# Kernel optimization log

Hardware: AMD Instinct MI355X
Metric: run time of the kernel (lower is better)

The kernel has to match this reference:

```python
import jax, jax.numpy as jnp
import numpy as np

EMBED_DIM = 1024
NUM_HEADS = 16
HEAD_DIM = EMBED_DIM // NUM_HEADS
EPS = 1e-6
B, T = 4, 8192


def setup_inputs() -> dict:
    key = jax.random.key(0)
    ks = jax.random.split(key, 11)
    s = 1.0 / np.sqrt(EMBED_DIM)
    inp = {
        'query': jax.random.normal(ks[0], (B, T, EMBED_DIM), jnp.float32),
        'key': jax.random.normal(ks[1], (B, T, EMBED_DIM), jnp.float32),
        'value': jax.random.normal(ks[2], (B, T, EMBED_DIM), jnp.float32),
        'Wq': jax.random.normal(ks[3], (EMBED_DIM, EMBED_DIM), jnp.float32) * s,
        'bq': jnp.zeros((EMBED_DIM,), jnp.float32),
        'Wk': jax.random.normal(ks[4], (EMBED_DIM, EMBED_DIM), jnp.float32) * s,
        'bk': jnp.zeros((EMBED_DIM,), jnp.float32),
        'Wv': jax.random.normal(ks[5], (EMBED_DIM, EMBED_DIM), jnp.float32) * s,
        'bv': jnp.zeros((EMBED_DIM,), jnp.float32),
        'Wo': jax.random.normal(ks[6], (EMBED_DIM, EMBED_DIM), jnp.float32) * s,
        'bo': jnp.zeros((EMBED_DIM,), jnp.float32),
    }
    return inp


def _feature_map(x):
    return jax.nn.elu(x) + 1.0


def reference(query, key, value, Wq, bq, Wk, bk, Wv, bv, Wo, bo):
    b, t, _ = query.shape
    # projections (torch Linear: x @ W.T + b)
    q = query @ Wq.T + bq
    k = key @ Wk.T + bk
    v = value @ Wv.T + bv
    # split heads -> (b, h, t, d)
    def split(x):
        return x.reshape(b, t, NUM_HEADS, HEAD_DIM).transpose(0, 2, 1, 3)
    q = _feature_map(split(q))
    k = _feature_map(split(k))
    v = split(v)
    k_sum = k.sum(axis=2)                                   # (b,h,d)
    denom = jnp.einsum('bhtd,bhd->bht', q, k_sum) + EPS     # (b,h,t)
    kv = jnp.einsum('bhtd,bhtv->bhdv', k, v)                # (b,h,d,d)
    out = jnp.einsum('bhtd,bhde->bhte', q, kv) / denom[..., None]
    out = out.transpose(0, 2, 1, 3).reshape(b, t, EMBED_DIM)
    return out @ Wo.T + bo
```

## Files before the change

### kernel.cpp

```cpp
#include <hip/hip_runtime.h>
#include <hip/hip_bf16.h>

typedef long long TLONG;
typedef float  f32x4_t  __attribute__((ext_vector_type(4)));
typedef short  s16x8_t  __attribute__((ext_vector_type(8)));
typedef short  s16x4_t  __attribute__((ext_vector_type(4)));
typedef __bf16 bf16x8_t __attribute__((ext_vector_type(8)));

#define MDIM 32768
#define NDIM 1024
#define KDIM 1024
#define EPSV 1e-6f

__device__ __forceinline__ unsigned short f2bf_bits(float f) {
  __hip_bfloat16 h = __float2bfloat16(f);
  return __builtin_bit_cast(unsigned short, h);
}
__device__ __forceinline__ float bf2f(unsigned short u) {
  unsigned int x = ((unsigned int)u) << 16;
  return __builtin_bit_cast(float, x);
}
__device__ __forceinline__ void load_lds16(const void* g, void* l) {
  __builtin_amdgcn_global_load_lds((const __attribute__((address_space(1))) void*)g,
                                   (__attribute__((address_space(3))) void*)l, 16, 0, 0);
}

__global__ __launch_bounds__(256) void convert_f32_bf16(
    const float* __restrict__ in, unsigned short* __restrict__ out, TLONG n) {
  TLONG i = ((TLONG)blockIdx.x * blockDim.x + threadIdx.x) * 8;
  const TLONG stride = (TLONG)gridDim.x * blockDim.x * 8;
  for (; i < n; i += stride) {
    f32x4_t a = *reinterpret_cast<const f32x4_t*>(in + i);
    f32x4_t b = *reinterpret_cast<const f32x4_t*>(in + i + 4);
    s16x8_t o;
    o[0] = (short)f2bf_bits(a[0]); o[1] = (short)f2bf_bits(a[1]);
    o[2] = (short)f2bf_bits(a[2]); o[3] = (short)f2bf_bits(a[3]);
    o[4] = (short)f2bf_bits(b[0]); o[5] = (short)f2bf_bits(b[1]);
    o[6] = (short)f2bf_bits(b[2]); o[7] = (short)f2bf_bits(b[3]);
    *reinterpret_cast<s16x8_t*>(out + i) = o;
  }
}

template <int FMAP, int OUT>
__global__ __launch_bounds__(256) void gemm_bt(
    const unsigned short* __restrict__ A, const unsigned short* __restrict__ W,
    const float* __restrict__ bias, void* __restrict__ Cout) {
  const int bid = blockIdx.x;
  const int swz = (bid & 7) * 256 + (bid >> 3);
  const int mt = swz >> 3;
  const int nt = swz & 7;

  const int tid = threadIdx.x;
  const int lane = tid & 63;
  const int w = tid >> 6;
  const int wr = w >> 1, wc = w & 1;
  const int l15 = lane & 15, lh = lane >> 4;

  __shared__ short sA[128 * 32];
  __shared__ short sB[128 * 32];

  f32x4_t acc[4][4];
#pragma unroll
  for (int m = 0; m < 4; ++m)
#pragma unroll
    for (int n = 0; n < 4; ++n) acc[m][n] = (f32x4_t)0.0f;

  const int arow0 = mt * 128;
  const int brow0 = nt * 128;

  for (int kt = 0; kt < KDIM / 32; ++kt) {
    const int k0 = kt * 32;
#pragma unroll
    for (int i = 0; i < 2; ++i) {
      const int c = i * 256 + tid;
      const int r = c >> 2, s = c & 3;
      const int sg = s ^ ((r >> 1) & 3);
      load_lds16(A + ((arow0 + r) * KDIM + k0 + sg * 8), &sA[c * 8]);
    }
#pragma unroll
    for (int i = 0; i < 2; ++i) {
      const int c = i * 256 + tid;
      const int r = c >> 2, s = c & 3;
      const int sg = s ^ ((r >> 1) & 3);
      load_lds16(W + ((brow0 + r) * KDIM + k0 + sg * 8), &sB[c * 8]);
    }
    __syncthreads();
    bf16x8_t a[4], b[4];
#pragma unroll
    for (int m = 0; m < 4; ++m) {
      const int rA = wr * 64 + m * 16 + l15;
      const int sl = lh ^ ((rA >> 1) & 3);
      a[m] = __builtin_bit_cast(bf16x8_t,
          *reinterpret_cast<const s16x8_t*>(&sA[rA * 32 + sl * 8]));
    }
#pragma unroll
    for (int n = 0; n < 4; ++n) {
      const int rB = wc * 64 + n * 16 + l15;
      const int sl = lh ^ ((rB >> 1) & 3);
      b[n] = __builtin_bit_cast(bf16x8_t,
          *reinterpret_cast<const s16x8_t*>(&sB[rB * 32 + sl * 8]));
    }
#pragma unroll
    for (int m = 0; m < 4; ++m)
#pragma unroll
      for (int n = 0; n < 4; ++n)
        acc[m][n] = __builtin_amdgcn_mfma_f32_16x16x32_bf16(a[m], b[n], acc[m][n], 0, 0, 0);
    __syncthreads();
  }

#pragma unroll
  for (int n = 0; n < 4; ++n) {
    const int col = nt * 128 + wc * 64 + n * 16 + l15;
    const float bv = bias[col];
#pragma unroll
    for (int m = 0; m < 4; ++m) {
      const int row0 = mt * 128 + wr * 64 + m * 16 + lh * 4;
      if (OUT == 2) {
        const int b = row0 >> 13, tl = row0 & 8191;
        const int h = col >> 6, d = col & 63;
        s16x4_t o;
#pragma unroll
        for (int j = 0; j < 4; ++j) {
          float v = acc[m][n][j] + bv;
          if (FMAP) v = (v > 0.0f) ? (v + 1.0f) : __expf(v);
          o[j] = (short)f2bf_bits(v);
        }
        *reinterpret_cast<s16x4_t*>(
            reinterpret_cast<unsigned short*>(Cout) +
            (((b * 16 + h) * 64 + d) * 8192 + tl)) = o;
      } else {
#pragma unroll
        for (int j = 0; j < 4; ++j) {
          float v = acc[m][n][j] + bv;
          if (FMAP) v = (v > 0.0f) ? (v + 1.0f) : __expf(v);
          if (OUT == 1)
            reinterpret_cast<float*>(Cout)[(row0 + j) * NDIM + col] = v;
          else
            reinterpret_cast<unsigned short*>(Cout)[(row0 + j) * NDIM + col] = f2bf_bits(v);
        }
      }
    }
  }
}

__global__ __launch_bounds__(256) void kv_ksum_mfma(
    const unsigned short* __restrict__ kT, const unsigned short* __restrict__ vT,
    float* __restrict__ kvT, float* __restrict__ ksum) {
  const int bid = blockIdx.x;
  const int bh = bid >> 4, ch = bid & 15;
  const int tid = threadIdx.x;
  const int lane = tid & 63, w = tid >> 6;
  const int l15 = lane & 15, lh = lane >> 4;
  const int dblk = (w >> 1) * 32, eblk = (w & 1) * 32;

  f32x4_t acc[2][2];
#pragma unroll
  for (int m = 0; m < 2; ++m)
#pragma unroll
    for (int n = 0; n < 2; ++n) acc[m][n] = (f32x4_t)0.0f;
  float ks0 = 0.f, ks1 = 0.f;

  const int tbase = ch * 512 + lh * 8;
  const unsigned short* ka = kT + (bh * 64 + dblk + l15) * 8192 + tbase;
  const unsigned short* va = vT + (bh * 64 + eblk + l15) * 8192 + tbase;

  for (int t0 = 0; t0 < 512; t0 += 32) {
    s16x8_t ar[2], br[2];
#pragma unroll
    for (int m = 0; m < 2; ++m)
      ar[m] = *reinterpret_cast<const s16x8_t*>(ka + m * 16 * 8192 + t0);
#pragma unroll
    for (int n = 0; n < 2; ++n)
      br[n] = *reinterpret_cast<const s16x8_t*>(va + n * 16 * 8192 + t0);
#pragma unroll
    for (int m = 0; m < 2; ++m)
#pragma unroll
      for (int n = 0; n < 2; ++n)
        acc[m][n] = __builtin_amdgcn_mfma_f32_16x16x32_bf16(
            __builtin_bit_cast(bf16x8_t, ar[m]),
            __builtin_bit_cast(bf16x8_t, br[n]), acc[m][n], 0, 0, 0);
    if (eblk == 0) {
#pragma unroll
      for (int i = 0; i < 8; ++i) ks0 += bf2f((unsigned short)ar[0][i]);
#pragma unroll
      for (int i = 0; i < 8; ++i) ks1 += bf2f((unsigned short)ar[1][i]);
    }
  }

  if (eblk == 0) {
    ks0 += __shfl_xor(ks0, 16); ks0 += __shfl_xor(ks0, 32);
    ks1 += __shfl_xor(ks1, 16); ks1 += __shfl_xor(ks1, 32);
    if (lh == 0) {
      atomicAdd(&ksum[bh * 64 + dblk + l15], ks0);
      atomicAdd(&ksum[bh * 64 + dblk + 16 + l15], ks1);
    }
  }
#pragma unroll
  for (int n = 0; n < 2; ++n) {
    const int e = eblk + n * 16 + l15;
#pragma unroll
    for (int m = 0; m < 2; ++m) {
      const int d0 = dblk + m * 16 + lh * 4;
#pragma unroll
      for (int j = 0; j < 4; ++j)
        atomicAdd(&kvT[(bh * 64 + e) * 64 + d0 + j], acc[m][n][j]);
    }
  }
}

__global__ __launch_bounds__(256) void attn_apply_kernel(
    const unsigned short* __restrict__ qf, const float* __restrict__ kvT,
    const float* __restrict__ ksum, unsigned short* __restrict__ att) {
  const int bid = blockIdx.x;
  const int swz = (bid & 7) * 256 + (bid >> 3);
  const int bh = swz >> 5;
  const int tile = swz & 31;
  const int b = bh >> 4, h = bh & 15;
  const int tid = threadIdx.x;
  const int lane = tid & 63, w = tid >> 6;
  const int l15 = lane & 15, lh = lane >> 4;

  float ksr[16];
#pragma unroll
  for (int i = 0; i < 16; ++i) ksr[i] = ksum[bh * 64 + lh * 16 + i];

  bf16x8_t bfrag[2][4];
#pragma unroll
  for (int ks2 = 0; ks2 < 2; ++ks2)
#pragma unroll
    for (int n = 0; n < 4; ++n) {
      const float* p = kvT + (bh * 64 + n * 16 + l15) * 64 + ks2 * 32 + lh * 8;
      f32x4_t p0 = *reinterpret_cast<const f32x4_t*>(p);
      f32x4_t p1 = *reinterpret_cast<const f32x4_t*>(p + 4);
      s16x8_t t;
      t[0] = (short)f2bf_bits(p0[0]); t[1] = (short)f2bf_bits(p0[1]);
      t[2] = (short)f2bf_bits(p0[2]); t[3] = (short)f2bf_bits(p0[3]);
      t[4] = (short)f2bf_bits(p1[0]); t[5] = (short)f2bf_bits(p1[1]);
      t[6] = (short)f2bf_bits(p1[2]); t[7] = (short)f2bf_bits(p1[3]);
      bfrag[ks2][n] = __builtin_bit_cast(bf16x8_t, t);
    }

  const int rbase = b * 8192 + tile * 256 + w * 64;
  f32x4_t acc[4][4];
#pragma unroll
  for (int m = 0; m < 4; ++m)
#pragma unroll
    for (int n = 0; n < 4; ++n) acc[m][n] = (f32x4_t)0.0f;
  float rden[4][4];

#pragma unroll
  for (int m = 0; m < 4; ++m) {
    const int row = rbase + m * 16 + l15;
    const unsigned short* qrow = qf + row * 1024 + h * 64;
    bf16x8_t afr[2];
#pragma unroll
    for (int ks2 = 0; ks2 < 2; ++ks2)
      afr[ks2] = __builtin_bit_cast(bf16x8_t,
          *reinterpret_cast<const s16x8_t*>(qrow + ks2 * 32 + lh * 8));
    s16x8_t qa = *reinterpret_cast<const s16x8_t*>(qrow + lh * 16);
    s16x8_t qb = *reinterpret_cast<const s16x8_t*>(qrow + lh * 16 + 8);
    float part = 0.f;
#pragma unroll
    for (int i = 0; i < 8; ++i) part += bf2f((unsigned short)qa[i]) * ksr[i];
#pragma unroll
    for (int i = 0; i < 8; ++i) part += bf2f((unsigned short)qb[i]) * ksr[8 + i];
    part += __shfl_xor(part, 16);
    part += __shfl_xor(part, 32);
#pragma unroll
    for (int j = 0; j < 4; ++j) {
      float dj = __shfl(part, lh * 4 + j);
      rden[m][j] = 1.0f / (dj + EPSV);
    }
#pragma unroll
    for (int ks2 = 0; ks2 < 2; ++ks2)
#pragma unroll
      for (int n = 0; n < 4; ++n)
        acc[m][n] = __builtin_amdgcn_mfma_f32_16x16x32_bf16(afr[ks2], bfrag[ks2][n], acc[m][n], 0, 0, 0);
  }

#pragma unroll
  for (int m = 0; m < 4; ++m)
#pragma unroll
    for (int n = 0; n < 4; ++n) {
      const int col = h * 64 + n * 16 + l15;
#pragma unroll
      for (int j = 0; j < 4; ++j) {
        const int row = rbase + m * 16 + lh * 4 + j;
        att[row * 1024 + col] = f2bf_bits(acc[m][n][j] * rden[m][j]);
      }
    }
}

extern "C" void kernel_launch(void* const* d_in, const int* in_sizes, int n_in,
                              void* d_out, int out_size, void* d_ws, size_t ws_size,
                              hipStream_t stream) {
  const float* query = (const float*)d_in[0];
  const float* key   = (const float*)d_in[1];
  const float* value = (const float*)d_in[2];
  const float* Wq = (const float*)d_in[3];
  const float* bq = (const float*)d_in[4];
  const float* Wk = (const float*)d_in[5];
  const float* bk = (const float*)d_in[6];
  const float* Wv = (const float*)d_in[7];
  const float* bv = (const float*)d_in[8];
  const float* Wo = (const float*)d_in[9];
  const float* bo = (const float*)d_in[10];
  float* out = (float*)d_out;

  if (ws_size < 277889024ULL) return;
  char* ws = (char*)d_ws;
  unsigned short* Vbf = (unsigned short*)(ws + 0);
  unsigned short* qf  = (unsigned short*)(ws + 67108864);
  unsigned short* kTf = (unsigned short*)(ws + 134217728);
  unsigned short* vTf = (unsigned short*)(ws + 201326592);
  unsigned short* Wqb = (unsigned short*)(ws + 268435456);
  unsigned short* Wkb = Wqb + 1048576;
  unsigned short* Wvb = Wkb + 1048576;
  unsigned short* Wob = Wvb + 1048576;
  float* kvT  = (float*)(ws + 276824064);
  float* ksum = (float*)(ws + 277872640);

  unsigned short* Qbf = (unsigned short*)d_out;
  unsigned short* Kbf = Qbf + 33554432;

  hipMemsetAsync(kvT, 0, (size_t)(64 * 64 * 64 + 64 * 64) * sizeof(float), stream);

  convert_f32_bf16<<<2048, 256, 0, stream>>>(query, Qbf, 33554432LL);
  convert_f32_bf16<<<2048, 256, 0, stream>>>(key,   Kbf, 33554432LL);
  convert_f32_bf16<<<2048, 256, 0, stream>>>(value, Vbf, 33554432LL);
  convert_f32_bf16<<<512, 256, 0, stream>>>(Wq, Wqb, 1048576LL);
  convert_f32_bf16<<<512, 256, 0, stream>>>(Wk, Wkb, 1048576LL);
  convert_f32_bf16<<<512, 256, 0, stream>>>(Wv, Wvb, 1048576LL);
  convert_f32_bf16<<<512, 256, 0, stream>>>(Wo, Wob, 1048576LL);

  gemm_bt<1, 0><<<2048, 256, 0, stream>>>(Qbf, Wqb, bq, qf);
  gemm_bt<1, 2><<<2048, 256, 0, stream>>>(Kbf, Wkb, bk, kTf);
  gemm_bt<0, 2><<<2048, 256, 0, stream>>>(Vbf, Wvb, bv, vTf);

  kv_ksum_mfma<<<1024, 256, 0, stream>>>(kTf, vTf, kvT, ksum);

  attn_apply_kernel<<<2048, 256, 0, stream>>>(qf, kvT, ksum, Vbf);

  gemm_bt<0, 1><<<2048, 256, 0, stream>>>(Vbf, Wob, bo, out);
}
```

Before: 674.3 us.

## Replace 128x128 GEMM with double-buffered 256x256 tile pipelined kernel

The projection GEMMs move from 128x128 tiles with K-step 32 and a single LDS buffer to 256x256 tiles with K-step 64, 512 threads, and a two-stage LDS double buffer. Loads for stage k+2 are issued asynchronously while MFMAs run, with explicit vmcnt waits, barriers and raised wave priority around the MFMA groups. The goals are more data reuse per LDS byte and overlap of global loads with compute. The cost is a 128KB LDS footprint and more accumulator registers, which limit occupancy, and the hand-tuned wait counts are fragile.

```diff
diff --git a/kernel.cpp b/kernel.cpp
--- a/kernel.cpp
+++ b/kernel.cpp
@@ -42,79 +42,114 @@
 }
 
 template <int FMAP, int OUT>
-__global__ __launch_bounds__(256) void gemm_bt(
+__global__ __launch_bounds__(512, 2) void gemm256(
     const unsigned short* __restrict__ A, const unsigned short* __restrict__ W,
     const float* __restrict__ bias, void* __restrict__ Cout) {
+  __shared__ short lds[65536];
   const int bid = blockIdx.x;
-  const int swz = (bid & 7) * 256 + (bid >> 3);
-  const int mt = swz >> 3;
-  const int nt = swz & 7;
+  const int swz = (bid & 7) * 64 + (bid >> 3);
+  const int mt = swz >> 2;
+  const int nt = swz & 3;
 
   const int tid = threadIdx.x;
   const int lane = tid & 63;
   const int w = tid >> 6;
-  const int wr = w >> 1, wc = w & 1;
+  const int wr = w >> 2, wc = w & 3;
   const int l15 = lane & 15, lh = lane >> 4;
 
-  __shared__ short sA[128 * 32];
-  __shared__ short sB[128 * 32];
-
-  f32x4_t acc[4][4];
-#pragma unroll
-  for (int m = 0; m < 4; ++m)
+  const int arow0 = mt * 256, brow0 = nt * 256;
+
+  auto stage = [&](const unsigned short* __restrict__ src, int lbase, int rowbase, int k0) {
+#pragma unroll
+    for (int i = 0; i < 4; ++i) {
+      const int c = i * 512 + tid;
+      const int r = c >> 3, ps = c & 7;
+      const int sg = ps ^ (r & 7);
+      load_lds16(src + (rowbase + r) * KDIM + k0 + sg * 8, &lds[lbase + c * 8]);
+    }
+  };
+
+  f32x4_t acc[8][4];
+#pragma unroll
+  for (int m = 0; m < 8; ++m)
 #pragma unroll
     for (int n = 0; n < 4; ++n) acc[m][n] = (f32x4_t)0.0f;
 
-  const int arow0 = mt * 128;
-  const int brow0 = nt * 128;
-
-  for (int kt = 0; kt < KDIM / 32; ++kt) {
-    const int k0 = kt * 32;
-#pragma unroll
-    for (int i = 0; i < 2; ++i) {
-      const int c = i * 256 + tid;
-      const int r = c >> 2, s = c & 3;
-      const int sg = s ^ ((r >> 1) & 3);
-      load_lds16(A + ((arow0 + r) * KDIM + k0 + sg * 8), &sA[c * 8]);
-    }
-#pragma unroll
-    for (int i = 0; i < 2; ++i) {
-      const int c = i * 256 + tid;
-      const int r = c >> 2, s = c & 3;
-      const int sg = s ^ ((r >> 1) & 3);
-      load_lds16(W + ((brow0 + r) * KDIM + k0 + sg * 8), &sB[c * 8]);
-    }
-    __syncthreads();
-    bf16x8_t a[4], b[4];
-#pragma unroll
-    for (int m = 0; m < 4; ++m) {
-      const int rA = wr * 64 + m * 16 + l15;
-      const int sl = lh ^ ((rA >> 1) & 3);
-      a[m] = __builtin_bit_cast(bf16x8_t,
-          *reinterpret_cast<const s16x8_t*>(&sA[rA * 32 + sl * 8]));
-    }
-#pragma unroll
-    for (int n = 0; n < 4; ++n) {
-      const int rB = wc * 64 + n * 16 + l15;
-      const int sl = lh ^ ((rB >> 1) & 3);
-      b[n] = __builtin_bit_cast(bf16x8_t,
-          *reinterpret_cast<const s16x8_t*>(&sB[rB * 32 + sl * 8]));
-    }
+  stage(A, 0, arow0, 0);
+  stage(W, 16384, brow0, 0);
+  stage(A, 32768, arow0, 64);
+  stage(W, 49152, brow0, 64);
+  asm volatile("s_waitcnt vmcnt(8)" ::: "memory");
+  __builtin_amdgcn_sched_barrier(0);
+  __builtin_amdgcn_s_barrier();
+
+  s16x8_t a0[4][2], a1[4][2], bf[4][2];
+
+  auto rdA = [&](int pb, int m, int ks) -> s16x8_t {
+    const int row = wr * 128 + m * 16 + l15;
+    const int off = pb + row * 64 + (((ks * 4 + lh) ^ (row & 7)) * 8);
+    return *reinterpret_cast<const s16x8_t*>(&lds[off]);
+  };
+  auto rdB = [&](int pb, int n, int ks) -> s16x8_t {
+    const int row = wc * 64 + n * 16 + l15;
+    const int off = pb + 16384 + row * 64 + (((ks * 4 + lh) ^ (row & 7)) * 8);
+    return *reinterpret_cast<const s16x8_t*>(&lds[off]);
+  };
+  auto quad = [&](s16x8_t (&af)[4][2], int mbase, int nlo) {
+    __builtin_amdgcn_s_setprio(1);
 #pragma unroll
     for (int m = 0; m < 4; ++m)
 #pragma unroll
-      for (int n = 0; n < 4; ++n)
-        acc[m][n] = __builtin_amdgcn_mfma_f32_16x16x32_bf16(a[m], b[n], acc[m][n], 0, 0, 0);
-    __syncthreads();
+      for (int n = 0; n < 2; ++n)
+#pragma unroll
+        for (int ks = 0; ks < 2; ++ks)
+          acc[mbase + m][nlo + n] = __builtin_amdgcn_mfma_f32_16x16x32_bf16(
+              __builtin_bit_cast(bf16x8_t, af[m][ks]),
+              __builtin_bit_cast(bf16x8_t, bf[nlo + n][ks]),
+              acc[mbase + m][nlo + n], 0, 0, 0);
+    __builtin_amdgcn_s_setprio(0);
+  };
+
+  for (int kt = 0; kt < 16; ++kt) {
+    const int pb = (kt & 1) * 32768;
+#pragma unroll
+    for (int m = 0; m < 4; ++m)
+#pragma unroll
+      for (int ks = 0; ks < 2; ++ks) a0[m][ks] = rdA(pb, m, ks);
+#pragma unroll
+    for (int n = 0; n < 4; ++n)
+#pragma unroll
+      for (int ks = 0; ks < 2; ++ks) bf[n][ks] = rdB(pb, n, ks);
+    quad(a0, 0, 0);
+#pragma unroll
+    for (int m = 0; m < 4; ++m)
+#pragma unroll
+      for (int ks = 0; ks < 2; ++ks) a1[m][ks] = rdA(pb, m + 4, ks);
+    quad(a0, 0, 2);
+    __builtin_amdgcn_sched_barrier(0);
+    asm volatile("s_waitcnt lgkmcnt(0)" ::: "memory");
+    __builtin_amdgcn_sched_barrier(0);
+    __builtin_amdgcn_s_barrier();
+    const int k2 = ((kt + 2) & 15) * 64;
+    stage(A, pb, arow0, k2);
+    quad(a1, 4, 0);
+    stage(W, pb + 16384, brow0, k2);
+    quad(a1, 4, 2);
+    if (kt < 15) {
+      __builtin_amdgcn_sched_barrier(0);
+      asm volatile("s_waitcnt vmcnt(8)" ::: "memory");
+      __builtin_amdgcn_sched_barrier(0);
+      __builtin_amdgcn_s_barrier();
+    }
   }
 
 #pragma unroll
   for (int n = 0; n < 4; ++n) {
-    const int col = nt * 128 + wc * 64 + n * 16 + l15;
+    const int col = nt * 256 + wc * 64 + n * 16 + l15;
     const float bv = bias[col];
 #pragma unroll
-    for (int m = 0; m < 4; ++m) {
-      const int row0 = mt * 128 + wr * 64 + m * 16 + lh * 4;
+    for (int m = 0; m < 8; ++m) {
+      const int row0 = mt * 256 + wr * 128 + m * 16 + lh * 4;
       if (OUT == 2) {
         const int b = row0 >> 13, tl = row0 & 8191;
         const int h = col >> 6, d = col & 63;
@@ -333,13 +368,13 @@
   convert_f32_bf16<<<512, 256, 0, stream>>>(Wv, Wvb, 1048576LL);
   convert_f32_bf16<<<512, 256, 0, stream>>>(Wo, Wob, 1048576LL);
 
-  gemm_bt<1, 0><<<2048, 256, 0, stream>>>(Qbf, Wqb, bq, qf);
-  gemm_bt<1, 2><<<2048, 256, 0, stream>>>(Kbf, Wkb, bk, kTf);
-  gemm_bt<0, 2><<<2048, 256, 0, stream>>>(Vbf, Wvb, bv, vTf);
+  gemm256<1, 0><<<512, 512, 0, stream>>>(Qbf, Wqb, bq, qf);
+  gemm256<1, 2><<<512, 512, 0, stream>>>(Kbf, Wkb, bk, kTf);
+  gemm256<0, 2><<<512, 512, 0, stream>>>(Vbf, Wvb, bv, vTf);
 
   kv_ksum_mfma<<<1024, 256, 0, stream>>>(kTf, vTf, kvT, ksum);
 
   attn_apply_kernel<<<2048, 256, 0, stream>>>(qf, kvT, ksum, Vbf);
 
-  gemm_bt<0, 1><<<2048, 256, 0, stream>>>(Vbf, Wob, bo, out);
-}
+  gemm256<0, 1><<<512, 512, 0, stream>>>(Vbf, Wob, bo, out);
+}
```

Measured after the change: 649.4 us. 1.04x faster.
